# Kernel optimization log

Measured on AMD Instinct MI355X. Metric: run time of the kernel, lower is better.

## Reference

```python
import jax, jax.numpy as jnp
import numpy as np

B, MSG, H, D, N = 64, 64, 512, 512, 2048


def setup_inputs() -> dict:
    key = jax.random.key(0)
    ks = jax.random.split(key, 20)
    s = 0.02
    return {
        "message": jax.random.normal(ks[0], (B, MSG), jnp.float32),
        "state": jax.random.normal(ks[1], (B, H), jnp.float32),
        "image": jax.random.normal(ks[2], (B, H), jnp.float32),
        "class_descriptors": jax.random.normal(ks[3], (N, D), jnp.float32),
        # GRUCell params (torch layout: gates ordered r, z, n)
        "w_ih": jax.random.normal(ks[4], (3 * H, MSG), jnp.float32) * s,
        "w_hh": jax.random.normal(ks[5], (3 * H, H), jnp.float32) * s,
        "b_ih": jax.random.normal(ks[6], (3 * H,), jnp.float32) * s,
        "b_hh": jax.random.normal(ks[7], (3 * H,), jnp.float32) * s,
        "w_stop": jax.random.normal(ks[8], (1, H), jnp.float32) * s,
        "b_stop": jax.random.normal(ks[9], (1,), jnp.float32) * s,
        "w_y1": jax.random.normal(ks[10], (H, H + D), jnp.float32) * s,
        "b_y1": jax.random.normal(ks[11], (H,), jnp.float32) * s,
        "w_y2": jax.random.normal(ks[12], (1, H), jnp.float32) * s,
        "b_y2": jax.random.normal(ks[13], (1,), jnp.float32) * s,
        "w_state": jax.random.normal(ks[14], (H, H), jnp.float32) * s,
        "b_state": jax.random.normal(ks[15], (H,), jnp.float32) * s,
        "w_desc": jax.random.normal(ks[16], (H, D), jnp.float32) * s,  # no bias
        "w_msg": jax.random.normal(ks[17], (MSG, H), jnp.float32) * s,
        "b_msg": jax.random.normal(ks[18], (MSG,), jnp.float32) * s,
    }


def _gru_cell(x, h, w_ih, w_hh, b_ih, b_hh):
    gi = x @ w_ih.T + b_ih  # [B, 3H]
    gh = h @ w_hh.T + b_hh
    i_r, i_z, i_n = jnp.split(gi, 3, axis=1)
    h_r, h_z, h_n = jnp.split(gh, 3, axis=1)
    r = jax.nn.sigmoid(i_r + h_r)
    z = jax.nn.sigmoid(i_z + h_z)
    n = jnp.tanh(i_n + r * h_n)
    return (1.0 - z) * n + z * h


def reference(message, state, image, class_descriptors,
              w_ih, w_hh, b_ih, b_hh, w_stop, b_stop,
              w_y1, b_y1, w_y2, b_y2, w_state, b_state,
              w_desc, w_msg, b_msg):
    b, h = state.shape
    n, d = class_descriptors.shape

    new_state = _gru_cell(message, state, w_ih, w_hh, b_ih, b_hh)  # [B, H]
    stop_dist = jax.nn.sigmoid(new_state @ w_stop.T + b_stop)  # [B, 1]
    stop_bit = jax.lax.stop_gradient(jnp.round(stop_dist))  # eval-mode path

    # build_state_descriptor_pairs (faithful to torch view semantics,
    # including the (B, H, N) -> (B*N, H) interleaved reshape of pair_left)
    pair_left = jnp.broadcast_to(new_state[:, :, None], (b, h, n)).reshape(b * n, h)
    pair_right = jnp.broadcast_to(class_descriptors[None], (b, n, d)).reshape(b * n, d)
    pairs = jnp.concatenate([pair_left, pair_right], axis=1)  # [B*N, H+D]

    y = jnp.clip(pairs @ w_y1.T + b_y1, 0.0, None)  # relu, [B*N, H]
    y = (y @ w_y2.T + b_y2).reshape(b, -1)  # [B, N]
    y_scores = jax.lax.stop_gradient(jax.nn.softmax(y, axis=1))

    # reweight_descriptors: softmax-weighted sum over descriptors
    descriptor_influence = jnp.einsum('bn,nd->bd', y_scores, class_descriptors)

    message_state = jnp.tanh(new_state @ w_state.T + b_state
                             + descriptor_influence @ w_desc.T)
    message_dist = jax.nn.sigmoid(message_state @ w_msg.T + b_msg)  # [B, MSG]
    outp_msg = jax.lax.stop_gradient(jnp.round(message_dist))

    return stop_bit, stop_dist, outp_msg, message_dist, y
```

## Files before the change

kernel.cpp:

```cpp
#include <hip/hip_runtime.h>


__device__ __forceinline__ float sigm(float x) { return 1.0f / (1.0f + expf(-x)); }

__device__ __forceinline__ void stage_pad68(float* dst, const float* src, int c) {
  *(float4*)&dst[(c >> 4) * 68 + (c & 15) * 4] = *(const float4*)&src[c * 4];
}

__global__ __launch_bounds__(512) void a_kernel(
    const float* __restrict__ msg, const float* __restrict__ st,
    const float* __restrict__ w_ih, const float* __restrict__ w_hh,
    const float* __restrict__ b_ih, const float* __restrict__ b_hh,
    const float* __restrict__ w_y1, const float* __restrict__ b_y1,
    const float* __restrict__ desc,
    float* __restrict__ ns, float* __restrict__ nsT, float* __restrict__ ws1,
    float* __restrict__ G) {
  __shared__ __align__(16) float sm[4352];
  const int t = threadIdx.x;
  const int blk = blockIdx.x;

  if (blk >= 576) {
    const int q = blk - 576;
    const int rr0 = (q >> 3) * 64;
    const int j0 = (q & 7) * 64;
    float* As = sm;
    float* Bs = sm + 2176;
    const int lrow = t >> 3;
    const int lk4 = (t & 7) * 4;
    const int tm2 = (t >> 4) * 2;
    const int tn4 = (t & 15) * 4;
    const float* aptr = desc + (rr0 + lrow) * 512 + lk4;
    const float* bptr = w_y1 + (j0 + lrow) * 1024 + 512 + lk4;
    float4 av = *(const float4*)aptr;
    float4 bv = *(const float4*)bptr;
    float acc[2][4] = {};
    for (int k0 = 0; k0 < 512; k0 += 32) {
      __syncthreads();
      As[(lk4 + 0) * 68 + lrow] = av.x; As[(lk4 + 1) * 68 + lrow] = av.y;
      As[(lk4 + 2) * 68 + lrow] = av.z; As[(lk4 + 3) * 68 + lrow] = av.w;
      Bs[(lk4 + 0) * 68 + lrow] = bv.x; Bs[(lk4 + 1) * 68 + lrow] = bv.y;
      Bs[(lk4 + 2) * 68 + lrow] = bv.z; Bs[(lk4 + 3) * 68 + lrow] = bv.w;
      __syncthreads();
      if (k0 + 32 < 512) {
        av = *(const float4*)(aptr + k0 + 32);
        bv = *(const float4*)(bptr + k0 + 32);
      }
      #pragma unroll
      for (int k = 0; k < 32; ++k) {
        float2 a = *(const float2*)&As[k * 68 + tm2];
        float4 b = *(const float4*)&Bs[k * 68 + tn4];
        acc[0][0] = fmaf(a.x, b.x, acc[0][0]); acc[0][1] = fmaf(a.x, b.y, acc[0][1]);
        acc[0][2] = fmaf(a.x, b.z, acc[0][2]); acc[0][3] = fmaf(a.x, b.w, acc[0][3]);
        acc[1][0] = fmaf(a.y, b.x, acc[1][0]); acc[1][1] = fmaf(a.y, b.y, acc[1][1]);
        acc[1][2] = fmaf(a.y, b.z, acc[1][2]); acc[1][3] = fmaf(a.y, b.w, acc[1][3]);
      }
    }
    float4 by = *(const float4*)&b_y1[j0 + tn4];
    float4 r0 = make_float4(acc[0][0] + by.x, acc[0][1] + by.y, acc[0][2] + by.z, acc[0][3] + by.w);
    float4 r1 = make_float4(acc[1][0] + by.x, acc[1][1] + by.y, acc[1][2] + by.z, acc[1][3] + by.w);
    *(float4*)&G[(rr0 + tm2) * 512 + j0 + tn4] = r0;
    *(float4*)&G[(rr0 + tm2 + 1) * 512 + j0 + tn4] = r1;
    return;
  }

  if (blk >= 512) {
    const int j = (blk - 512) * 8 + (t >> 6);
    const int lane = t & 63;
    const float* row = w_y1 + j * 1024 + lane * 8;
    float4 a = *(const float4*)&row[0];
    float4 b = *(const float4*)&row[4];
    float acc = a.x + a.y + a.z + a.w + b.x + b.y + b.z + b.w;
    #pragma unroll
    for (int m = 1; m < 64; m <<= 1) acc += __shfl_xor(acc, m, 64);
    if (lane == 0) ws1[j] = acc;
    return;
  }

  const int h = blk;
  float* sHr = sm;
  float* sHz = sm + 544;
  float* sHn = sm + 1088;
  float* sIr = sm + 1632;
  float* sIz = sm + 1696;
  float* sIn = sm + 1760;
  if (t < 128)      stage_pad68(sHr, w_hh + h * 512, t);
  else if (t < 256) stage_pad68(sHz, w_hh + (h + 512) * 512, t - 128);
  else if (t < 384) stage_pad68(sHn, w_hh + (h + 1024) * 512, t - 256);
  else if (t < 400) ((float4*)sIr)[t - 384] = ((const float4*)(w_ih + h * 64))[t - 384];
  else if (t < 416) ((float4*)sIz)[t - 400] = ((const float4*)(w_ih + (h + 512) * 64))[t - 400];
  else if (t < 432) ((float4*)sIn)[t - 416] = ((const float4*)(w_ih + (h + 1024) * 64))[t - 416];
  __syncthreads();
  const int bi = t >> 3, kg = t & 7;
  float pr = 0.f, pz = 0.f, pin = 0.f, phn = 0.f;
  {
    const float* mrow = msg + bi * 64 + kg * 8;
    const float* ir = &sIr[kg * 8];
    const float* iz = &sIz[kg * 8];
    const float* in_ = &sIn[kg * 8];
    #pragma unroll
    for (int i = 0; i < 2; ++i) {
      float4 x = *(const float4*)&mrow[i * 4];
      float4 wr = *(const float4*)&ir[i * 4];
      float4 wz = *(const float4*)&iz[i * 4];
      float4 wn = *(const float4*)&in_[i * 4];
      pr = fmaf(x.x, wr.x, pr); pr = fmaf(x.y, wr.y, pr); pr = fmaf(x.z, wr.z, pr); pr = fmaf(x.w, wr.w, pr);
      pz = fmaf(x.x, wz.x, pz); pz = fmaf(x.y, wz.y, pz); pz = fmaf(x.z, wz.z, pz); pz = fmaf(x.w, wz.w, pz);
      pin = fmaf(x.x, wn.x, pin); pin = fmaf(x.y, wn.y, pin); pin = fmaf(x.z, wn.z, pin); pin = fmaf(x.w, wn.w, pin);
    }
  }
  {
    const float* srow = st + bi * 512 + kg * 64;
    const float* hr = &sHr[kg * 68];
    const float* hz = &sHz[kg * 68];
    const float* hn = &sHn[kg * 68];
    #pragma unroll
    for (int i = 0; i < 16; ++i) {
      float4 x = *(const float4*)&srow[i * 4];
      float4 wr = *(const float4*)&hr[i * 4];
      float4 wz = *(const float4*)&hz[i * 4];
      float4 wn = *(const float4*)&hn[i * 4];
      pr = fmaf(x.x, wr.x, pr); pr = fmaf(x.y, wr.y, pr); pr = fmaf(x.z, wr.z, pr); pr = fmaf(x.w, wr.w, pr);
      pz = fmaf(x.x, wz.x, pz); pz = fmaf(x.y, wz.y, pz); pz = fmaf(x.z, wz.z, pz); pz = fmaf(x.w, wz.w, pz);
      phn = fmaf(x.x, wn.x, phn); phn = fmaf(x.y, wn.y, phn); phn = fmaf(x.z, wn.z, phn); phn = fmaf(x.w, wn.w, phn);
    }
  }
  pr += __shfl_xor(pr, 1, 8); pr += __shfl_xor(pr, 2, 8); pr += __shfl_xor(pr, 4, 8);
  pz += __shfl_xor(pz, 1, 8); pz += __shfl_xor(pz, 2, 8); pz += __shfl_xor(pz, 4, 8);
  pin += __shfl_xor(pin, 1, 8); pin += __shfl_xor(pin, 2, 8); pin += __shfl_xor(pin, 4, 8);
  phn += __shfl_xor(phn, 1, 8); phn += __shfl_xor(phn, 2, 8); phn += __shfl_xor(phn, 4, 8);
  if ((t & 7) == 0) {
    float r = sigm(pr + b_ih[h] + b_hh[h]);
    float z = sigm(pz + b_ih[h + 512] + b_hh[h + 512]);
    float n = tanhf(pin + b_ih[h + 1024] + r * (phn + b_hh[h + 1024]));
    float hp = st[bi * 512 + h];
    float v = (1.0f - z) * n + z * hp;
    ns[bi * 512 + h] = v;
    nsT[h * 64 + bi] = v;
  }
}

__global__ __launch_bounds__(256) void ystop_kernel(
    const float* __restrict__ nsT, const float* __restrict__ ws1,
    const float* __restrict__ G, const float* __restrict__ w_y2,
    const float* __restrict__ b_y2, float* __restrict__ yf,
    const float* __restrict__ ns, const float* __restrict__ w_stop,
    const float* __restrict__ b_stop, float* __restrict__ out_bit,
    float* __restrict__ out_dist, float* __restrict__ di) {
  const int t = threadIdx.x;
  if (blockIdx.x > 2048) {
    const int idx = (blockIdx.x - 2049) * 512 + t * 2;
    *(float2*)&di[idx] = make_float2(0.f, 0.f);
    return;
  }
  if (blockIdx.x == 2048) {
    const int bi = t >> 2, kg = t & 3;
    const float* row = ns + bi * 512 + kg * 128;
    const float* wrow = w_stop + kg * 128;
    float acc = 0.f;
    #pragma unroll
    for (int i = 0; i < 32; ++i) {
      float4 r = *(const float4*)&row[i * 4];
      float4 w = *(const float4*)&wrow[i * 4];
      acc = fmaf(r.x, w.x, acc); acc = fmaf(r.y, w.y, acc);
      acc = fmaf(r.z, w.z, acc); acc = fmaf(r.w, w.w, acc);
    }
    acc += __shfl_xor(acc, 1, 4); acc += __shfl_xor(acc, 2, 4);
    if (kg == 0) {
      float sd = sigm(acc + b_stop[0]);
      out_dist[bi] = sd;
      out_bit[bi] = rintf(sd);
    }
    return;
  }
  const int rr = blockIdx.x;
  __shared__ __align__(16) float sG[512], sW1[512], sW2[512];
  __shared__ float sp[4 * 72];
  if (t < 128) {
    ((float4*)sG)[t] = ((const float4*)(G + rr * 512))[t];
    ((float4*)sW2)[t] = ((const float4*)w_y2)[t];
  } else {
    ((float4*)sW1)[t - 128] = ((const float4*)ws1)[t - 128];
  }
  __syncthreads();
  const int bi = t & 63, jq = t >> 6;
  const float v = nsT[(rr >> 2) * 64 + bi];
  float acc = 0.0f;
  const float* g = sG + jq * 128;
  const float* w1 = sW1 + jq * 128;
  const float* w2 = sW2 + jq * 128;
  #pragma unroll 4
  for (int j = 0; j < 128; j += 4) {
    float4 gv = *(const float4*)&g[j];
    float4 a1 = *(const float4*)&w1[j];
    float4 a2 = *(const float4*)&w2[j];
    acc = fmaf(a2.x, fmaxf(fmaf(v, a1.x, gv.x), 0.0f), acc);
    acc = fmaf(a2.y, fmaxf(fmaf(v, a1.y, gv.y), 0.0f), acc);
    acc = fmaf(a2.z, fmaxf(fmaf(v, a1.z, gv.z), 0.0f), acc);
    acc = fmaf(a2.w, fmaxf(fmaf(v, a1.w, gv.w), 0.0f), acc);
  }
  sp[jq * 72 + bi] = acc;
  __syncthreads();
  if (t < 64) {
    float y = sp[t] + sp[72 + t] + sp[144 + t] + sp[216 + t] + b_y2[0];
    yf[t * 2048 + rr] = y;
  }
}

__global__ __launch_bounds__(256) void softmax_kernel(
    const float* __restrict__ yf, float* __restrict__ out_y,
    float* __restrict__ mxv, float* __restrict__ sumv) {
  const int bi = blockIdx.x;
  const int t = threadIdx.x;
  __shared__ float sy[2048];
  __shared__ float red[256];
  float lmax = -3.0e38f;
  for (int i = t; i < 2048; i += 256) {
    float v = yf[bi * 2048 + i];
    sy[i] = v;
    out_y[bi * 2048 + i] = v;
    lmax = fmaxf(lmax, v);
  }
  red[t] = lmax;
  __syncthreads();
  for (int s = 128; s > 0; s >>= 1) {
    if (t < s) red[t] = fmaxf(red[t], red[t + s]);
    __syncthreads();
  }
  const float mx = red[0];
  __syncthreads();
  float lsum = 0.0f;
  for (int i = t; i < 2048; i += 256) lsum += expf(sy[i] - mx);
  red[t] = lsum;
  __syncthreads();
  for (int s = 128; s > 0; s >>= 1) {
    if (t < s) red[t] += red[t + s];
    __syncthreads();
  }
  if (t == 0) { mxv[bi] = mx; sumv[bi] = red[0]; }
}

__global__ __launch_bounds__(256) void di_part_kernel(
    const float* __restrict__ yf, const float* __restrict__ mxv,
    const float* __restrict__ desc, float* __restrict__ di) {
  __shared__ __align__(16) float sE[64 * 66];
  __shared__ __align__(16) float sD[64 * 68];
  __shared__ float sMx[64];
  const int d0 = blockIdx.x * 64;
  const int n0 = blockIdx.y * 64;
  const int t = threadIdx.x;
  if (t < 64) sMx[t] = mxv[t];
  __syncthreads();
  {
    const int bi = t >> 2;
    const float m = sMx[bi];
    #pragma unroll
    for (int i = 0; i < 4; ++i) {
      const int kq = (t & 3) * 4 + i * 16;
      float4 av = *(const float4*)&yf[bi * 2048 + n0 + kq];
      sE[(kq + 0) * 66 + bi] = expf(av.x - m);
      sE[(kq + 1) * 66 + bi] = expf(av.y - m);
      sE[(kq + 2) * 66 + bi] = expf(av.z - m);
      sE[(kq + 3) * 66 + bi] = expf(av.w - m);
    }
    #pragma unroll
    for (int i = 0; i < 4; ++i) {
      const int nn = (t >> 4) + i * 16;
      const int dq = (t & 15) * 4;
      *(float4*)&sD[nn * 68 + dq] = *(const float4*)&desc[(n0 + nn) * 512 + d0 + dq];
    }
  }
  __syncthreads();
  const int bi0 = (t >> 4) * 4;
  const int dd0 = (t & 15) * 4;
  float acc[4][4] = {};
  #pragma unroll 8
  for (int nn = 0; nn < 64; ++nn) {
    float4 a = *(const float4*)&sE[nn * 66 + bi0];
    float4 b = *(const float4*)&sD[nn * 68 + dd0];
    acc[0][0] = fmaf(a.x, b.x, acc[0][0]); acc[0][1] = fmaf(a.x, b.y, acc[0][1]);
    acc[0][2] = fmaf(a.x, b.z, acc[0][2]); acc[0][3] = fmaf(a.x, b.w, acc[0][3]);
    acc[1][0] = fmaf(a.y, b.x, acc[1][0]); acc[1][1] = fmaf(a.y, b.y, acc[1][1]);
    acc[1][2] = fmaf(a.y, b.z, acc[1][2]); acc[1][3] = fmaf(a.y, b.w, acc[1][3]);
    acc[2][0] = fmaf(a.z, b.x, acc[2][0]); acc[2][1] = fmaf(a.z, b.y, acc[2][1]);
    acc[2][2] = fmaf(a.z, b.z, acc[2][2]); acc[2][3] = fmaf(a.z, b.w, acc[2][3]);
    acc[3][0] = fmaf(a.w, b.x, acc[3][0]); acc[3][1] = fmaf(a.w, b.y, acc[3][1]);
    acc[3][2] = fmaf(a.w, b.z, acc[3][2]); acc[3][3] = fmaf(a.w, b.w, acc[3][3]);
  }
  #pragma unroll
  for (int i = 0; i < 4; ++i)
    #pragma unroll
    for (int j = 0; j < 4; ++j)
      atomicAdd(&di[(bi0 + i) * 512 + d0 + dd0 + j], acc[i][j]);
}

__global__ __launch_bounds__(512) void ms_kernel(
    const float* __restrict__ ns, const float* __restrict__ di,
    const float* __restrict__ sumv,
    const float* __restrict__ w_state, const float* __restrict__ b_state,
    const float* __restrict__ w_desc, float* __restrict__ ms) {
  const int hj = blockIdx.x;
  const int t = threadIdx.x;
  __shared__ __align__(16) float sWs[544], sWd[544];
  __shared__ float sInv[64];
  if (t < 128)      stage_pad68(sWs, w_state + hj * 512, t);
  else if (t < 256) stage_pad68(sWd, w_desc + hj * 512, t - 128);
  else if (t < 320) sInv[t - 256] = 1.0f / sumv[t - 256];
  __syncthreads();
  const int bi = t >> 3, kg = t & 7;
  const float* nr = ns + bi * 512 + kg * 64;
  const float* dr = di + bi * 512 + kg * 64;
  const float* wsp = &sWs[kg * 68];
  const float* wdp = &sWd[kg * 68];
  float accs = 0.f, accd = 0.f;
  #pragma unroll
  for (int i = 0; i < 16; ++i) {
    float4 a = *(const float4*)&nr[i * 4];
    float4 w = *(const float4*)&wsp[i * 4];
    float4 b = *(const float4*)&dr[i * 4];
    float4 u = *(const float4*)&wdp[i * 4];
    accs = fmaf(a.x, w.x, accs); accs = fmaf(a.y, w.y, accs);
    accs = fmaf(a.z, w.z, accs); accs = fmaf(a.w, w.w, accs);
    accd = fmaf(b.x, u.x, accd); accd = fmaf(b.y, u.y, accd);
    accd = fmaf(b.z, u.z, accd); accd = fmaf(b.w, u.w, accd);
  }
  accs += __shfl_xor(accs, 1, 8); accs += __shfl_xor(accs, 2, 8); accs += __shfl_xor(accs, 4, 8);
  accd += __shfl_xor(accd, 1, 8); accd += __shfl_xor(accd, 2, 8); accd += __shfl_xor(accd, 4, 8);
  if ((t & 7) == 0)
    ms[bi * 512 + hj] = tanhf(accs + accd * sInv[bi] + b_state[hj]);
}

__global__ __launch_bounds__(512) void msg_kernel(
    const float* __restrict__ ms, const float* __restrict__ w_msg,
    const float* __restrict__ b_msg, float* __restrict__ out_msg,
    float* __restrict__ out_msgdist) {
  const int m = blockIdx.x;
  const int t = threadIdx.x;
  __shared__ __align__(16) float sW[544];
  if (t < 128) stage_pad68(sW, w_msg + m * 512, t);
  __syncthreads();
  const int bi = t >> 3, kg = t & 7;
  const float* row = ms + bi * 512 + kg * 64;
  const float* wp = &sW[kg * 68];
  float acc = 0.f;
  #pragma unroll
  for (int i = 0; i < 16; ++i) {
    float4 a = *(const float4*)&row[i * 4];
    float4 w = *(const float4*)&wp[i * 4];
    acc = fmaf(a.x, w.x, acc); acc = fmaf(a.y, w.y, acc);
    acc = fmaf(a.z, w.z, acc); acc = fmaf(a.w, w.w, acc);
  }
  acc += __shfl_xor(acc, 1, 8); acc += __shfl_xor(acc, 2, 8); acc += __shfl_xor(acc, 4, 8);
  if ((t & 7) == 0) {
    float md = sigm(acc + b_msg[m]);
    out_msgdist[bi * 64 + m] = md;
    out_msg[bi * 64 + m] = rintf(md);
  }
}

extern "C" void kernel_launch(void* const* d_in, const int* in_sizes, int n_in,
                              void* d_out, int out_size, void* d_ws, size_t ws_size,
                              hipStream_t stream) {
  (void)in_sizes; (void)n_in; (void)out_size; (void)ws_size;
  const float* message = (const float*)d_in[0];
  const float* state   = (const float*)d_in[1];
  const float* desc    = (const float*)d_in[3];
  const float* w_ih    = (const float*)d_in[4];
  const float* w_hh    = (const float*)d_in[5];
  const float* b_ih    = (const float*)d_in[6];
  const float* b_hh    = (const float*)d_in[7];
  const float* w_stop  = (const float*)d_in[8];
  const float* b_stop  = (const float*)d_in[9];
  const float* w_y1    = (const float*)d_in[10];
  const float* b_y1    = (const float*)d_in[11];
  const float* w_y2    = (const float*)d_in[12];
  const float* b_y2    = (const float*)d_in[13];
  const float* w_state = (const float*)d_in[14];
  const float* b_state = (const float*)d_in[15];
  const float* w_desc  = (const float*)d_in[16];
  const float* w_msg   = (const float*)d_in[17];
  const float* b_msg   = (const float*)d_in[18];

  float* out = (float*)d_out;
  float* out_stopbit  = out;
  float* out_stopdist = out + 64;
  float* out_msg      = out + 128;
  float* out_msgdist  = out + 4224;
  float* out_y        = out + 8320;

  char* ws = (char*)d_ws;
  float* ns   = (float*)(ws);
  float* nsT  = (float*)(ws + 131072);
  float* ws1  = (float*)(ws + 262144);
  float* G    = (float*)(ws + 264192);
  float* yf   = (float*)(ws + 4458496);
  float* di   = (float*)(ws + 4982784);
  float* ms   = (float*)(ws + 5113856);
  float* mxv  = (float*)(ws + 5244928);
  float* sumv = (float*)(ws + 5245184);

  a_kernel<<<832, 512, 0, stream>>>(message, state, w_ih, w_hh, b_ih, b_hh,
                                    w_y1, b_y1, desc, ns, nsT, ws1, G);
  ystop_kernel<<<2113, 256, 0, stream>>>(nsT, ws1, G, w_y2, b_y2, yf,
                                         ns, w_stop, b_stop, out_stopbit,
                                         out_stopdist, di);
  softmax_kernel<<<64, 256, 0, stream>>>(yf, out_y, mxv, sumv);
  di_part_kernel<<<dim3(8, 32), 256, 0, stream>>>(yf, mxv, desc, di);
  ms_kernel<<<512, 512, 0, stream>>>(ns, di, sumv, w_state, b_state, w_desc, ms);
  msg_kernel<<<64, 512, 0, stream>>>(ms, w_msg, b_msg, out_msg, out_msgdist);
}
```

Before: 207.5 us.

## Split descriptor GEMM into separate 256-thread kernel with swizzled LDS tiles

Moves the desc×W_y1 GEMM that produces G out of the fused GRU/ws1 kernel into its own kernel. The new kernel uses 32×64 tiles with 256 threads and an XOR-swizzled B tile in LDS to avoid bank conflicts. The GRU kernel no longer reserves the large shared buffer it used to share with the GEMM blocks. This adds a kernel launch and removes the overlap between GEMM blocks and GRU blocks that the fused grid allowed.

```diff
diff --git a/kernel.cpp b/kernel.cpp
--- a/kernel.cpp
+++ b/kernel.cpp
@@ -7,64 +7,15 @@
   *(float4*)&dst[(c >> 4) * 68 + (c & 15) * 4] = *(const float4*)&src[c * 4];
 }
 
-__global__ __launch_bounds__(512) void a_kernel(
+__global__ __launch_bounds__(512) void gruws1_kernel(
     const float* __restrict__ msg, const float* __restrict__ st,
     const float* __restrict__ w_ih, const float* __restrict__ w_hh,
     const float* __restrict__ b_ih, const float* __restrict__ b_hh,
-    const float* __restrict__ w_y1, const float* __restrict__ b_y1,
-    const float* __restrict__ desc,
-    float* __restrict__ ns, float* __restrict__ nsT, float* __restrict__ ws1,
-    float* __restrict__ G) {
-  __shared__ __align__(16) float sm[4352];
-  const int t = threadIdx.x;
-  const int blk = blockIdx.x;
-
-  if (blk >= 576) {
-    const int q = blk - 576;
-    const int rr0 = (q >> 3) * 64;
-    const int j0 = (q & 7) * 64;
-    float* As = sm;
-    float* Bs = sm + 2176;
-    const int lrow = t >> 3;
-    const int lk4 = (t & 7) * 4;
-    const int tm2 = (t >> 4) * 2;
-    const int tn4 = (t & 15) * 4;
-    const float* aptr = desc + (rr0 + lrow) * 512 + lk4;
-    const float* bptr = w_y1 + (j0 + lrow) * 1024 + 512 + lk4;
-    float4 av = *(const float4*)aptr;
-    float4 bv = *(const float4*)bptr;
-    float acc[2][4] = {};
-    for (int k0 = 0; k0 < 512; k0 += 32) {
-      __syncthreads();
-      As[(lk4 + 0) * 68 + lrow] = av.x; As[(lk4 + 1) * 68 + lrow] = av.y;
-      As[(lk4 + 2) * 68 + lrow] = av.z; As[(lk4 + 3) * 68 + lrow] = av.w;
-      Bs[(lk4 + 0) * 68 + lrow] = bv.x; Bs[(lk4 + 1) * 68 + lrow] = bv.y;
-      Bs[(lk4 + 2) * 68 + lrow] = bv.z; Bs[(lk4 + 3) * 68 + lrow] = bv.w;
-      __syncthreads();
-      if (k0 + 32 < 512) {
-        av = *(const float4*)(aptr + k0 + 32);
-        bv = *(const float4*)(bptr + k0 + 32);
-      }
-      #pragma unroll
-      for (int k = 0; k < 32; ++k) {
-        float2 a = *(const float2*)&As[k * 68 + tm2];
-        float4 b = *(const float4*)&Bs[k * 68 + tn4];
-        acc[0][0] = fmaf(a.x, b.x, acc[0][0]); acc[0][1] = fmaf(a.x, b.y, acc[0][1]);
-        acc[0][2] = fmaf(a.x, b.z, acc[0][2]); acc[0][3] = fmaf(a.x, b.w, acc[0][3]);
-        acc[1][0] = fmaf(a.y, b.x, acc[1][0]); acc[1][1] = fmaf(a.y, b.y, acc[1][1]);
-        acc[1][2] = fmaf(a.y, b.z, acc[1][2]); acc[1][3] = fmaf(a.y, b.w, acc[1][3]);
-      }
-    }
-    float4 by = *(const float4*)&b_y1[j0 + tn4];
-    float4 r0 = make_float4(acc[0][0] + by.x, acc[0][1] + by.y, acc[0][2] + by.z, acc[0][3] + by.w);
-    float4 r1 = make_float4(acc[1][0] + by.x, acc[1][1] + by.y, acc[1][2] + by.z, acc[1][3] + by.w);
-    *(float4*)&G[(rr0 + tm2) * 512 + j0 + tn4] = r0;
-    *(float4*)&G[(rr0 + tm2 + 1) * 512 + j0 + tn4] = r1;
-    return;
-  }
-
-  if (blk >= 512) {
-    const int j = (blk - 512) * 8 + (t >> 6);
+    const float* __restrict__ w_y1,
+    float* __restrict__ ns, float* __restrict__ nsT, float* __restrict__ ws1) {
+  const int t = threadIdx.x;
+  if (blockIdx.x >= 512) {
+    const int j = (blockIdx.x - 512) * 8 + (t >> 6);
     const int lane = t & 63;
     const float* row = w_y1 + j * 1024 + lane * 8;
     float4 a = *(const float4*)&row[0];
@@ -75,14 +26,9 @@
     if (lane == 0) ws1[j] = acc;
     return;
   }
-
-  const int h = blk;
-  float* sHr = sm;
-  float* sHz = sm + 544;
-  float* sHn = sm + 1088;
-  float* sIr = sm + 1632;
-  float* sIz = sm + 1696;
-  float* sIn = sm + 1760;
+  const int h = blockIdx.x;
+  __shared__ __align__(16) float sHr[544], sHz[544], sHn[544];
+  __shared__ __align__(16) float sIr[64], sIz[64], sIn[64];
   if (t < 128)      stage_pad68(sHr, w_hh + h * 512, t);
   else if (t < 256) stage_pad68(sHz, w_hh + (h + 512) * 512, t - 128);
   else if (t < 384) stage_pad68(sHn, w_hh + (h + 1024) * 512, t - 256);
@@ -137,6 +83,59 @@
     ns[bi * 512 + h] = v;
     nsT[h * 64 + bi] = v;
   }
+}
+
+__global__ __launch_bounds__(256, 2) void g_kernel(
+    const float* __restrict__ desc, const float* __restrict__ w_y1,
+    const float* __restrict__ b_y1, float* __restrict__ G) {
+  __shared__ __align__(16) float As[32 * 34];
+  __shared__ __align__(16) float Bs[32 * 68];
+  const int rr0 = blockIdx.x * 32;
+  const int j0 = blockIdx.y * 64;
+  const int t = threadIdx.x;
+  const int lrow = t >> 3;
+  const int lk4 = (t & 7) * 4;
+  const int swz = (t & 7) << 2;
+  const int tm2 = (t >> 4) * 2;
+  const int tn4 = (t & 15) * 4;
+  const int bc0 = lrow ^ swz;
+  const float* aptr = desc + (rr0 + lrow) * 512 + lk4;
+  const float* bptr0 = w_y1 + (j0 + lrow) * 1024 + 512 + lk4;
+  const float* bptr1 = bptr0 + 32 * 1024;
+  float4 av = *(const float4*)aptr;
+  float4 bv0 = *(const float4*)bptr0;
+  float4 bv1 = *(const float4*)bptr1;
+  float acc[2][4] = {};
+  for (int k0 = 0; k0 < 512; k0 += 32) {
+    __syncthreads();
+    As[(lk4 + 0) * 34 + lrow] = av.x; As[(lk4 + 1) * 34 + lrow] = av.y;
+    As[(lk4 + 2) * 34 + lrow] = av.z; As[(lk4 + 3) * 34 + lrow] = av.w;
+    Bs[(lk4 + 0) * 68 + bc0] = bv0.x; Bs[(lk4 + 1) * 68 + bc0] = bv0.y;
+    Bs[(lk4 + 2) * 68 + bc0] = bv0.z; Bs[(lk4 + 3) * 68 + bc0] = bv0.w;
+    Bs[(lk4 + 0) * 68 + bc0 + 32] = bv1.x; Bs[(lk4 + 1) * 68 + bc0 + 32] = bv1.y;
+    Bs[(lk4 + 2) * 68 + bc0 + 32] = bv1.z; Bs[(lk4 + 3) * 68 + bc0 + 32] = bv1.w;
+    __syncthreads();
+    if (k0 + 32 < 512) {
+      av = *(const float4*)(aptr + k0 + 32);
+      bv0 = *(const float4*)(bptr0 + k0 + 32);
+      bv1 = *(const float4*)(bptr1 + k0 + 32);
+    }
+    #pragma unroll
+    for (int k = 0; k < 32; ++k) {
+      float a0 = As[k * 34 + tm2];
+      float a1 = As[k * 34 + tm2 + 1];
+      float4 b = *(const float4*)&Bs[k * 68 + (tn4 ^ ((k >> 2) << 2))];
+      acc[0][0] = fmaf(a0, b.x, acc[0][0]); acc[0][1] = fmaf(a0, b.y, acc[0][1]);
+      acc[0][2] = fmaf(a0, b.z, acc[0][2]); acc[0][3] = fmaf(a0, b.w, acc[0][3]);
+      acc[1][0] = fmaf(a1, b.x, acc[1][0]); acc[1][1] = fmaf(a1, b.y, acc[1][1]);
+      acc[1][2] = fmaf(a1, b.z, acc[1][2]); acc[1][3] = fmaf(a1, b.w, acc[1][3]);
+    }
+  }
+  float4 by = *(const float4*)&b_y1[j0 + tn4];
+  float4 r0 = make_float4(acc[0][0] + by.x, acc[0][1] + by.y, acc[0][2] + by.z, acc[0][3] + by.w);
+  float4 r1 = make_float4(acc[1][0] + by.x, acc[1][1] + by.y, acc[1][2] + by.z, acc[1][3] + by.w);
+  *(float4*)&G[(rr0 + tm2) * 512 + j0 + tn4] = r0;
+  *(float4*)&G[(rr0 + tm2 + 1) * 512 + j0 + tn4] = r1;
 }
 
 __global__ __launch_bounds__(256) void ystop_kernel(
@@ -398,8 +397,9 @@
   float* mxv  = (float*)(ws + 5244928);
   float* sumv = (float*)(ws + 5245184);
 
-  a_kernel<<<832, 512, 0, stream>>>(message, state, w_ih, w_hh, b_ih, b_hh,
-                                    w_y1, b_y1, desc, ns, nsT, ws1, G);
+  gruws1_kernel<<<576, 512, 0, stream>>>(message, state, w_ih, w_hh, b_ih, b_hh,
+                                         w_y1, ns, nsT, ws1);
+  g_kernel<<<dim3(64, 8), 256, 0, stream>>>(desc, w_y1, b_y1, G);
   ystop_kernel<<<2113, 256, 0, stream>>>(nsT, ws1, G, w_y2, b_y2, yf,
                                          ns, w_stop, b_stop, out_stopbit,
                                          out_stopdist, di);
```

Result: no change. 208.8 us (+0.7%).
